# Performance work log

Measured on AMD Instinct MI355X. Metric: run time of the kernel, lower is better.

## Reference

```python
import jax, jax.numpy as jnp
import numpy as np


def _pairwise_sqdist(a, b):
    # a: [B,N,3], b: [B,M,3] -> [B,N,M] squared L2 distances
    a2 = jnp.sum(a * a, axis=-1)            # [B,N]
    b2 = jnp.sum(b * b, axis=-1)            # [B,M]
    ab = jnp.einsum('bnd,bmd->bnm', a, b)   # [B,N,M]
    d = a2[:, :, None] + b2[:, None, :] - 2.0 * ab
    return jnp.maximum(d, 0.0)


def setup_inputs() -> dict:
    key = jax.random.key(0)
    k1, k2 = jax.random.split(key)
    B, N, M = 4, 8192, 8192
    p1 = jax.random.normal(k1, (B, N, 3), dtype=jnp.float32)
    p2 = jax.random.normal(k2, (B, M, 3), dtype=jnp.float32)
    return {"p1": p1, "p2": p2}


def reference(p1, p2):
    # chamfer_3DDist: squared L2 NN distances both directions, then mean of each
    d = _pairwise_sqdist(p1, p2)   # [B,N,M]
    d1 = jnp.min(d, axis=2)        # [B,N] nearest p2 for each p1 point
    d2 = jnp.min(d, axis=1)        # [B,M] nearest p1 for each p2 point
    return jnp.mean(d1) + jnp.mean(d2)
```

## Files before the change

kernel.cpp:

```cpp
#include <hip/hip_runtime.h>
#include <float.h>


typedef float v2f __attribute__((ext_vector_type(2)));
typedef float v4f __attribute__((ext_vector_type(4)));

#define BLK   256
#define QPT   8
#define QPB   (BLK * QPT)
#define BATCH 4
#define NPTS  8192
#define NCH   32
#define CHUNK (NPTS / NCH)
#define QTILES (NPTS / QPB)
#define GRID  (2 * BATCH * QTILES * NCH)
#define TOTQ  (2 * BATCH * NPTS)
#define WS_NEED ((size_t)NCH * TOTQ * sizeof(float))

__global__ void zero_out_kernel(float* out) { out[0] = 0.f; }

__global__ __launch_bounds__(BLK) void cd_chunk_kernel(
    const float* __restrict__ p1, const float* __restrict__ p2,
    float* __restrict__ part)
{
    __shared__ v4f pts[CHUNK];
    int bid    = blockIdx.x;
    int mchunk = bid & (NCH - 1);
    int qt     = (bid >> 5) & (QTILES - 1);
    int batch  = (bid >> 7) & (BATCH - 1);
    int dir    = bid >> 9;

    const float* qbase = (dir == 0 ? p1 : p2) + (size_t)batch * NPTS * 3;
    const float* dbase = (dir == 0 ? p2 : p1) + (size_t)batch * NPTS * 3;

    int tid = threadIdx.x;

    if (tid < CHUNK / 4) {
        int t4 = tid * 4;
        const float* s = dbase + (size_t)(mchunk * CHUNK + t4) * 3;
        float4 f0 = *(const float4*)(s);
        float4 f1 = *(const float4*)(s + 4);
        float4 f2 = *(const float4*)(s + 8);
        float x0 = f0.x, y0 = f0.y, z0 = f0.z;
        float x1 = f0.w, y1 = f1.x, z1 = f1.y;
        float x2 = f1.z, y2 = f1.w, z2 = f2.x;
        float x3 = f2.y, y3 = f2.z, z3 = f2.w;
        float w0 = -0.5f * (x0*x0 + y0*y0 + z0*z0);
        float w1 = -0.5f * (x1*x1 + y1*y1 + z1*z1);
        float w2 = -0.5f * (x2*x2 + y2*y2 + z2*z2);
        float w3 = -0.5f * (x3*x3 + y3*y3 + z3*z3);
        pts[4*tid + 0] = (v4f){x0, x1, y0, y1};
        pts[4*tid + 1] = (v4f){z0, z1, w0, w1};
        pts[4*tid + 2] = (v4f){x2, x3, y2, y3};
        pts[4*tid + 3] = (v4f){z2, z3, w2, w3};
    }

    v2f qx2[QPT], qy2[QPT], qz2[QPT];
    float qn[QPT];
    #pragma unroll
    for (int k = 0; k < QPT; ++k) {
        int q = qt * QPB + k * BLK + tid;
        const float* s = qbase + (size_t)q * 3;
        float qx = s[0], qy = s[1], qz = s[2];
        qx2[k] = (v2f){qx, qx};
        qy2[k] = (v2f){qy, qy};
        qz2[k] = (v2f){qz, qz};
        qn[k] = qx * qx + qy * qy + qz * qz;
    }
    __syncthreads();

    v2f acc0[QPT], acc1[QPT];
    #pragma unroll
    for (int k = 0; k < QPT; ++k) {
        acc0[k] = (v2f){-FLT_MAX, -FLT_MAX};
        acc1[k] = (v2f){-FLT_MAX, -FLT_MAX};
    }

    #pragma unroll 2
    for (int m = 0; m < CHUNK / 2; m += 2) {
        v4f u0 = pts[2*m + 0];
        v4f v0 = pts[2*m + 1];
        v4f u1 = pts[2*m + 2];
        v4f v1 = pts[2*m + 3];
        v2f X0 = __builtin_shufflevector(u0, u0, 0, 1);
        v2f Y0 = __builtin_shufflevector(u0, u0, 2, 3);
        v2f Z0 = __builtin_shufflevector(v0, v0, 0, 1);
        v2f W0 = __builtin_shufflevector(v0, v0, 2, 3);
        v2f X1 = __builtin_shufflevector(u1, u1, 0, 1);
        v2f Y1 = __builtin_shufflevector(u1, u1, 2, 3);
        v2f Z1 = __builtin_shufflevector(v1, v1, 0, 1);
        v2f W1 = __builtin_shufflevector(v1, v1, 2, 3);
        #pragma unroll
        for (int k = 0; k < QPT; ++k) {
            v2f s0 = __builtin_elementwise_fma(qz2[k], Z0,
                      __builtin_elementwise_fma(qy2[k], Y0,
                       __builtin_elementwise_fma(qx2[k], X0, W0)));
            acc0[k] = __builtin_elementwise_max(acc0[k], s0);
            v2f s1 = __builtin_elementwise_fma(qz2[k], Z1,
                      __builtin_elementwise_fma(qy2[k], Y1,
                       __builtin_elementwise_fma(qx2[k], X1, W1)));
            acc1[k] = __builtin_elementwise_max(acc1[k], s1);
        }
    }

    unsigned qid = (unsigned)(dir * (BATCH * NPTS) + batch * NPTS + qt * QPB + tid);
    float* prow = part + (size_t)mchunk * TOTQ;
    #pragma unroll
    for (int k = 0; k < QPT; ++k) {
        float mx = fmaxf(fmaxf(acc0[k].x, acc0[k].y), fmaxf(acc1[k].x, acc1[k].y));
        float d = fmaxf(qn[k] - 2.f * mx, 0.f);
        prow[qid + k * BLK] = d;
    }
}

__global__ __launch_bounds__(BLK) void min_sum_kernel(
    const float* __restrict__ part, float* __restrict__ out, float scale)
{
    int qid = blockIdx.x * BLK + threadIdx.x;
    float v = FLT_MAX;
    #pragma unroll 8
    for (int m = 0; m < NCH; ++m)
        v = fminf(v, part[(size_t)m * TOTQ + qid]);
    for (int off = 32; off > 0; off >>= 1) v += __shfl_down(v, off, 64);
    __shared__ float wsum[BLK / 64];
    int lane = threadIdx.x & 63, wid = threadIdx.x >> 6;
    if (lane == 0) wsum[wid] = v;
    __syncthreads();
    if (threadIdx.x == 0) {
        float t = 0.f;
        for (int w = 0; w < BLK / 64; ++w) t += wsum[w];
        atomicAdd(out, t * scale);
    }
}

__global__ __launch_bounds__(BLK) void init_kernel(unsigned* mins, float* out, int n) {
    int i = blockIdx.x * BLK + threadIdx.x;
    if (i < n) mins[i] = 0x7F7FFFFFu;
    if (i == 0) out[0] = 0.f;
}

__global__ __launch_bounds__(BLK) void cd_chunk_atomic_kernel(
    const float* __restrict__ p1, const float* __restrict__ p2,
    unsigned* __restrict__ mins)
{
    __shared__ v4f pts[CHUNK];
    int bid    = blockIdx.x;
    int mchunk = bid & (NCH - 1);
    int qt     = (bid >> 5) & (QTILES - 1);
    int batch  = (bid >> 7) & (BATCH - 1);
    int dir    = bid >> 9;

    const float* qbase = (dir == 0 ? p1 : p2) + (size_t)batch * NPTS * 3;
    const float* dbase = (dir == 0 ? p2 : p1) + (size_t)batch * NPTS * 3;
    int tid = threadIdx.x;

    if (tid < CHUNK / 4) {
        int t4 = tid * 4;
        const float* s = dbase + (size_t)(mchunk * CHUNK + t4) * 3;
        float4 f0 = *(const float4*)(s);
        float4 f1 = *(const float4*)(s + 4);
        float4 f2 = *(const float4*)(s + 8);
        float x0 = f0.x, y0 = f0.y, z0 = f0.z;
        float x1 = f0.w, y1 = f1.x, z1 = f1.y;
        float x2 = f1.z, y2 = f1.w, z2 = f2.x;
        float x3 = f2.y, y3 = f2.z, z3 = f2.w;
        float w0 = -0.5f * (x0*x0 + y0*y0 + z0*z0);
        float w1 = -0.5f * (x1*x1 + y1*y1 + z1*z1);
        float w2 = -0.5f * (x2*x2 + y2*y2 + z2*z2);
        float w3 = -0.5f * (x3*x3 + y3*y3 + z3*z3);
        pts[4*tid + 0] = (v4f){x0, x1, y0, y1};
        pts[4*tid + 1] = (v4f){z0, z1, w0, w1};
        pts[4*tid + 2] = (v4f){x2, x3, y2, y3};
        pts[4*tid + 3] = (v4f){z2, z3, w2, w3};
    }

    v2f qx2[QPT], qy2[QPT], qz2[QPT];
    float qn[QPT];
    #pragma unroll
    for (int k = 0; k < QPT; ++k) {
        int q = qt * QPB + k * BLK + tid;
        const float* s = qbase + (size_t)q * 3;
        float qx = s[0], qy = s[1], qz = s[2];
        qx2[k] = (v2f){qx, qx}; qy2[k] = (v2f){qy, qy}; qz2[k] = (v2f){qz, qz};
        qn[k] = qx * qx + qy * qy + qz * qz;
    }
    __syncthreads();

    v2f acc0[QPT], acc1[QPT];
    #pragma unroll
    for (int k = 0; k < QPT; ++k) {
        acc0[k] = (v2f){-FLT_MAX, -FLT_MAX};
        acc1[k] = (v2f){-FLT_MAX, -FLT_MAX};
    }
    #pragma unroll 2
    for (int m = 0; m < CHUNK / 2; m += 2) {
        v4f u0 = pts[2*m + 0], v0 = pts[2*m + 1];
        v4f u1 = pts[2*m + 2], v1 = pts[2*m + 3];
        v2f X0 = __builtin_shufflevector(u0, u0, 0, 1);
        v2f Y0 = __builtin_shufflevector(u0, u0, 2, 3);
        v2f Z0 = __builtin_shufflevector(v0, v0, 0, 1);
        v2f W0 = __builtin_shufflevector(v0, v0, 2, 3);
        v2f X1 = __builtin_shufflevector(u1, u1, 0, 1);
        v2f Y1 = __builtin_shufflevector(u1, u1, 2, 3);
        v2f Z1 = __builtin_shufflevector(v1, v1, 0, 1);
        v2f W1 = __builtin_shufflevector(v1, v1, 2, 3);
        #pragma unroll
        for (int k = 0; k < QPT; ++k) {
            v2f s0 = __builtin_elementwise_fma(qz2[k], Z0,
                      __builtin_elementwise_fma(qy2[k], Y0,
                       __builtin_elementwise_fma(qx2[k], X0, W0)));
            acc0[k] = __builtin_elementwise_max(acc0[k], s0);
            v2f s1 = __builtin_elementwise_fma(qz2[k], Z1,
                      __builtin_elementwise_fma(qy2[k], Y1,
                       __builtin_elementwise_fma(qx2[k], X1, W1)));
            acc1[k] = __builtin_elementwise_max(acc1[k], s1);
        }
    }
    unsigned qid = (unsigned)(dir * (BATCH * NPTS) + batch * NPTS + qt * QPB + tid);
    #pragma unroll
    for (int k = 0; k < QPT; ++k) {
        float mx = fmaxf(fmaxf(acc0[k].x, acc0[k].y), fmaxf(acc1[k].x, acc1[k].y));
        float d = fmaxf(qn[k] - 2.f * mx, 0.f);
        atomicMin(&mins[qid + k * BLK], __float_as_uint(d));
    }
}

__global__ __launch_bounds__(BLK) void sum_kernel(
    const unsigned* __restrict__ mins, float* __restrict__ out, int n, float scale)
{
    int i = blockIdx.x * BLK + threadIdx.x;
    int stride = gridDim.x * BLK;
    float v = 0.f;
    for (int idx = i; idx < n; idx += stride) v += __uint_as_float(mins[idx]);
    for (int off = 32; off > 0; off >>= 1) v += __shfl_down(v, off, 64);
    __shared__ float wsum[BLK / 64];
    int lane = threadIdx.x & 63, wid = threadIdx.x >> 6;
    if (lane == 0) wsum[wid] = v;
    __syncthreads();
    if (threadIdx.x == 0) {
        float t = 0.f;
        for (int w = 0; w < BLK / 64; ++w) t += wsum[w];
        atomicAdd(out, t * scale);
    }
}

extern "C" void kernel_launch(void* const* d_in, const int* in_sizes, int n_in,
                              void* d_out, int out_size, void* d_ws, size_t ws_size,
                              hipStream_t stream) {
    const float* p1 = (const float*)d_in[0];
    const float* p2 = (const float*)d_in[1];
    float* out = (float*)d_out;

    if (ws_size >= WS_NEED) {
        float* part = (float*)d_ws;
        zero_out_kernel<<<1, 1, 0, stream>>>(out);
        cd_chunk_kernel<<<GRID, BLK, 0, stream>>>(p1, p2, part);
        min_sum_kernel<<<TOTQ / BLK, BLK, 0, stream>>>(part, out,
                                                       1.f / (float)(BATCH * NPTS));
    } else {
        unsigned* mins = (unsigned*)d_ws;
        init_kernel<<<TOTQ / BLK, BLK, 0, stream>>>(mins, out, TOTQ);
        cd_chunk_atomic_kernel<<<GRID, BLK, 0, stream>>>(p1, p2, mins);
        sum_kernel<<<64, BLK, 0, stream>>>(mins, out, TOTQ, 1.f / (float)(BATCH * NPTS));
    }
}
```

Before: 107.2 us.

## Compute pairwise distance scores with bf16 split-precision MFMA instead of packed FMA

Replaces the packed-FP32 FMA distance loop with a 32x32x16 bf16 MFMA. Each coordinate and the norm term are split into high and low bf16 parts, so one K=16 matrix product approximates the dot product plus the norm offset with near-fp32 accuracy. Query tiles shrink to 128 per block and the database is split into 8 chunks, which also cuts the partial-min workspace and the reduction reads. The cost is bf16 rounding error in the scores, per-tile cross-lane shuffles to reduce the MFMA output, and 16 separate MFMA-max steps per tile.

```diff
diff --git a/kernel.cpp b/kernel.cpp
--- a/kernel.cpp
+++ b/kernel.cpp
@@ -2,42 +2,190 @@
 #include <float.h>
 
 
+typedef short sh8   __attribute__((ext_vector_type(8)));
+typedef float f32x16 __attribute__((ext_vector_type(16)));
+
+#define BLK   256
+#define BATCH 4
+#define NPTS  8192
+#define PCH   8
+#define PCHUNK (NPTS / PCH)
+#define QPB   128
+#define QTILES (NPTS / QPB)
+#define GRID  (2 * BATCH * QTILES * PCH)
+#define TOTQ  (2 * BATCH * NPTS)
+#define WS_NEED ((size_t)PCH * TOTQ * sizeof(float))
+#define ONEBF 0x3F80
+
+__device__ __forceinline__ short f2bf(float f) {
+    unsigned u = __float_as_uint(f);
+    unsigned r = (u + 0x7FFFu + ((u >> 16) & 1u)) >> 16;
+    return (short)r;
+}
+__device__ __forceinline__ float bf2f(short h) {
+    return __uint_as_float(((unsigned)(unsigned short)h) << 16);
+}
+
+__global__ void zero_out_kernel(float* out) { out[0] = 0.f; }
+
+__global__ __launch_bounds__(BLK) void cd_mfma_kernel(
+    const float* __restrict__ p1, const float* __restrict__ p2,
+    float* __restrict__ part)
+{
+    __shared__ uint4 ptsB[PCHUNK * 2];
+
+    int bid    = blockIdx.x;
+    int pchunk = bid & (PCH - 1);
+    int qt     = (bid >> 3) & (QTILES - 1);
+    int batch  = (bid >> 9) & (BATCH - 1);
+    int dir    = bid >> 11;
+
+    const float* qbase = (dir == 0 ? p1 : p2) + (size_t)batch * NPTS * 3;
+    const float* dbase = (dir == 0 ? p2 : p1) + (size_t)batch * NPTS * 3;
+
+    int tid  = threadIdx.x;
+    int wave = tid >> 6;
+    int lane = tid & 63;
+
+    {
+        int t4 = tid * 4;
+        const float* s = dbase + (size_t)(pchunk * PCHUNK + t4) * 3;
+        float4 f0 = *(const float4*)(s);
+        float4 f1 = *(const float4*)(s + 4);
+        float4 f2 = *(const float4*)(s + 8);
+        float px[4] = {f0.x, f0.w, f1.z, f2.y};
+        float py[4] = {f0.y, f1.x, f1.w, f2.z};
+        float pz[4] = {f0.z, f1.y, f2.x, f2.w};
+        #pragma unroll
+        for (int i = 0; i < 4; ++i) {
+            float x = px[i], y = py[i], z = pz[i];
+            short hx = f2bf(x), hy = f2bf(y), hz = f2bf(z);
+            short lx = f2bf(x - bf2f(hx));
+            short ly = f2bf(y - bf2f(hy));
+            short lz = f2bf(z - bf2f(hz));
+            float w = -0.5f * (x * x + y * y + z * z);
+            short wh = f2bf(w);
+            short wl = f2bf(w - bf2f(wh));
+            unsigned uhx = (unsigned short)hx, uhy = (unsigned short)hy, uhz = (unsigned short)hz;
+            unsigned ulx = (unsigned short)lx, uly = (unsigned short)ly, ulz = (unsigned short)lz;
+            ptsB[(t4 + i) * 2 + 0] = make_uint4(
+                uhx | (uhy << 16), uhz | (uhx << 16),
+                uhy | (uhz << 16), ulx | (uly << 16));
+            ptsB[(t4 + i) * 2 + 1] = make_uint4(
+                ulz | (ulx << 16), uly | (ulz << 16),
+                (unsigned)(unsigned short)wh | ((unsigned)(unsigned short)wl << 16),
+                ((unsigned)ONEBF) | (((unsigned)ONEBF) << 16));
+        }
+    }
+
+    sh8 afrag;
+    {
+        int q = qt * QPB + wave * 32 + (lane & 31);
+        const float* s = qbase + (size_t)q * 3;
+        float x = s[0], y = s[1], z = s[2];
+        short hx = f2bf(x), hy = f2bf(y), hz = f2bf(z);
+        short lx = f2bf(x - bf2f(hx));
+        short ly = f2bf(y - bf2f(hy));
+        short lz = f2bf(z - bf2f(hz));
+        float w = -0.5f * (x * x + y * y + z * z);
+        short nh = f2bf(w);
+        short nl = f2bf(w - bf2f(nh));
+        int h = lane >> 5;
+        afrag[0] = h ? hz : hx;
+        afrag[1] = h ? lx : hy;
+        afrag[2] = h ? ly : hz;
+        afrag[3] = h ? lz : lx;
+        afrag[4] = h ? (short)ONEBF : ly;
+        afrag[5] = h ? (short)ONEBF : lz;
+        afrag[6] = h ? nh : hx;
+        afrag[7] = h ? nl : hy;
+    }
+    __syncthreads();
+
+    f32x16 zc;
+    f32x16 runmax;
+    #pragma unroll
+    for (int i = 0; i < 16; ++i) { zc[i] = 0.f; runmax[i] = -FLT_MAX; }
+
+    const sh8* bptr = (const sh8*)ptsB;
+    int boff = (lane & 31) * 2 + (lane >> 5);
+
+    #pragma unroll 4
+    for (int t = 0; t < PCHUNK / 32; ++t) {
+        sh8 bfrag = bptr[t * 64 + boff];
+        f32x16 acc = __builtin_amdgcn_mfma_f32_32x32x16_bf16(afrag, bfrag, zc, 0, 0, 0);
+        runmax = __builtin_elementwise_max(runmax, acc);
+    }
+
+    #pragma unroll
+    for (int step = 1; step <= 16; step <<= 1) {
+        f32x16 o;
+        #pragma unroll
+        for (int i = 0; i < 16; ++i) o[i] = __shfl_xor(runmax[i], step, 64);
+        runmax = __builtin_elementwise_max(runmax, o);
+    }
+
+    if ((lane & 31) == 0) {
+        int half = lane >> 5;
+        int qglob = dir * (BATCH * NPTS) + batch * NPTS + qt * QPB + wave * 32;
+        float* prow = part + (size_t)pchunk * TOTQ + qglob;
+        #pragma unroll
+        for (int reg = 0; reg < 16; ++reg) {
+            int r = (reg & 3) + 8 * (reg >> 2) + 4 * half;
+            float d = fmaxf(-2.f * runmax[reg], 0.f);
+            prow[r] = d;
+        }
+    }
+}
+
+__global__ __launch_bounds__(BLK) void min_sum_kernel(
+    const float* __restrict__ part, float* __restrict__ out, float scale)
+{
+    int qid = blockIdx.x * BLK + threadIdx.x;
+    float v = FLT_MAX;
+    #pragma unroll
+    for (int m = 0; m < PCH; ++m)
+        v = fminf(v, part[(size_t)m * TOTQ + qid]);
+    for (int off = 32; off > 0; off >>= 1) v += __shfl_down(v, off, 64);
+    __shared__ float wsum[BLK / 64];
+    int lane = threadIdx.x & 63, wid = threadIdx.x >> 6;
+    if (lane == 0) wsum[wid] = v;
+    __syncthreads();
+    if (threadIdx.x == 0) {
+        float t = 0.f;
+        for (int w = 0; w < BLK / 64; ++w) t += wsum[w];
+        atomicAdd(out, t * scale);
+    }
+}
+
 typedef float v2f __attribute__((ext_vector_type(2)));
 typedef float v4f __attribute__((ext_vector_type(4)));
-
-#define BLK   256
-#define QPT   8
-#define QPB   (BLK * QPT)
-#define BATCH 4
-#define NPTS  8192
-#define NCH   32
-#define CHUNK (NPTS / NCH)
-#define QTILES (NPTS / QPB)
-#define GRID  (2 * BATCH * QTILES * NCH)
-#define TOTQ  (2 * BATCH * NPTS)
-#define WS_NEED ((size_t)NCH * TOTQ * sizeof(float))
-
-__global__ void zero_out_kernel(float* out) { out[0] = 0.f; }
-
-__global__ __launch_bounds__(BLK) void cd_chunk_kernel(
+#define FQPT   8
+#define FNCH   32
+#define FCHUNK (NPTS / FNCH)
+
+__global__ __launch_bounds__(BLK) void init_kernel(unsigned* mins, float* out, int n) {
+    int i = blockIdx.x * BLK + threadIdx.x;
+    if (i < n) mins[i] = 0x7F7FFFFFu;
+    if (i == 0) out[0] = 0.f;
+}
+
+__global__ __launch_bounds__(BLK) void cd_chunk_atomic_kernel(
     const float* __restrict__ p1, const float* __restrict__ p2,
-    float* __restrict__ part)
-{
-    __shared__ v4f pts[CHUNK];
+    unsigned* __restrict__ mins)
+{
+    __shared__ v4f pts[FCHUNK];
     int bid    = blockIdx.x;
-    int mchunk = bid & (NCH - 1);
-    int qt     = (bid >> 5) & (QTILES - 1);
+    int mchunk = bid & (FNCH - 1);
+    int qt     = (bid >> 5) & 3;
     int batch  = (bid >> 7) & (BATCH - 1);
     int dir    = bid >> 9;
-
     const float* qbase = (dir == 0 ? p1 : p2) + (size_t)batch * NPTS * 3;
     const float* dbase = (dir == 0 ? p2 : p1) + (size_t)batch * NPTS * 3;
-
     int tid = threadIdx.x;
-
-    if (tid < CHUNK / 4) {
+    if (tid < FCHUNK / 4) {
         int t4 = tid * 4;
-        const float* s = dbase + (size_t)(mchunk * CHUNK + t4) * 3;
+        const float* s = dbase + (size_t)(mchunk * FCHUNK + t4) * 3;
         float4 f0 = *(const float4*)(s);
         float4 f1 = *(const float4*)(s + 4);
         float4 f2 = *(const float4*)(s + 8);
@@ -54,146 +202,25 @@
         pts[4*tid + 2] = (v4f){x2, x3, y2, y3};
         pts[4*tid + 3] = (v4f){z2, z3, w2, w3};
     }
-
-    v2f qx2[QPT], qy2[QPT], qz2[QPT];
-    float qn[QPT];
-    #pragma unroll
-    for (int k = 0; k < QPT; ++k) {
-        int q = qt * QPB + k * BLK + tid;
-        const float* s = qbase + (size_t)q * 3;
-        float qx = s[0], qy = s[1], qz = s[2];
-        qx2[k] = (v2f){qx, qx};
-        qy2[k] = (v2f){qy, qy};
-        qz2[k] = (v2f){qz, qz};
-        qn[k] = qx * qx + qy * qy + qz * qz;
-    }
-    __syncthreads();
-
-    v2f acc0[QPT], acc1[QPT];
-    #pragma unroll
-    for (int k = 0; k < QPT; ++k) {
-        acc0[k] = (v2f){-FLT_MAX, -FLT_MAX};
-        acc1[k] = (v2f){-FLT_MAX, -FLT_MAX};
-    }
-
-    #pragma unroll 2
-    for (int m = 0; m < CHUNK / 2; m += 2) {
-        v4f u0 = pts[2*m + 0];
-        v4f v0 = pts[2*m + 1];
-        v4f u1 = pts[2*m + 2];
-        v4f v1 = pts[2*m + 3];
-        v2f X0 = __builtin_shufflevector(u0, u0, 0, 1);
-        v2f Y0 = __builtin_shufflevector(u0, u0, 2, 3);
-        v2f Z0 = __builtin_shufflevector(v0, v0, 0, 1);
-        v2f W0 = __builtin_shufflevector(v0, v0, 2, 3);
-        v2f X1 = __builtin_shufflevector(u1, u1, 0, 1);
-        v2f Y1 = __builtin_shufflevector(u1, u1, 2, 3);
-        v2f Z1 = __builtin_shufflevector(v1, v1, 0, 1);
-        v2f W1 = __builtin_shufflevector(v1, v1, 2, 3);
-        #pragma unroll
-        for (int k = 0; k < QPT; ++k) {
-            v2f s0 = __builtin_elementwise_fma(qz2[k], Z0,
-                      __builtin_elementwise_fma(qy2[k], Y0,
-                       __builtin_elementwise_fma(qx2[k], X0, W0)));
-            acc0[k] = __builtin_elementwise_max(acc0[k], s0);
-            v2f s1 = __builtin_elementwise_fma(qz2[k], Z1,
-                      __builtin_elementwise_fma(qy2[k], Y1,
-                       __builtin_elementwise_fma(qx2[k], X1, W1)));
-            acc1[k] = __builtin_elementwise_max(acc1[k], s1);
-        }
-    }
-
-    unsigned qid = (unsigned)(dir * (BATCH * NPTS) + batch * NPTS + qt * QPB + tid);
-    float* prow = part + (size_t)mchunk * TOTQ;
-    #pragma unroll
-    for (int k = 0; k < QPT; ++k) {
-        float mx = fmaxf(fmaxf(acc0[k].x, acc0[k].y), fmaxf(acc1[k].x, acc1[k].y));
-        float d = fmaxf(qn[k] - 2.f * mx, 0.f);
-        prow[qid + k * BLK] = d;
-    }
-}
-
-__global__ __launch_bounds__(BLK) void min_sum_kernel(
-    const float* __restrict__ part, float* __restrict__ out, float scale)
-{
-    int qid = blockIdx.x * BLK + threadIdx.x;
-    float v = FLT_MAX;
-    #pragma unroll 8
-    for (int m = 0; m < NCH; ++m)
-        v = fminf(v, part[(size_t)m * TOTQ + qid]);
-    for (int off = 32; off > 0; off >>= 1) v += __shfl_down(v, off, 64);
-    __shared__ float wsum[BLK / 64];
-    int lane = threadIdx.x & 63, wid = threadIdx.x >> 6;
-    if (lane == 0) wsum[wid] = v;
-    __syncthreads();
-    if (threadIdx.x == 0) {
-        float t = 0.f;
-        for (int w = 0; w < BLK / 64; ++w) t += wsum[w];
-        atomicAdd(out, t * scale);
-    }
-}
-
-__global__ __launch_bounds__(BLK) void init_kernel(unsigned* mins, float* out, int n) {
-    int i = blockIdx.x * BLK + threadIdx.x;
-    if (i < n) mins[i] = 0x7F7FFFFFu;
-    if (i == 0) out[0] = 0.f;
-}
-
-__global__ __launch_bounds__(BLK) void cd_chunk_atomic_kernel(
-    const float* __restrict__ p1, const float* __restrict__ p2,
-    unsigned* __restrict__ mins)
-{
-    __shared__ v4f pts[CHUNK];
-    int bid    = blockIdx.x;
-    int mchunk = bid & (NCH - 1);
-    int qt     = (bid >> 5) & (QTILES - 1);
-    int batch  = (bid >> 7) & (BATCH - 1);
-    int dir    = bid >> 9;
-
-    const float* qbase = (dir == 0 ? p1 : p2) + (size_t)batch * NPTS * 3;
-    const float* dbase = (dir == 0 ? p2 : p1) + (size_t)batch * NPTS * 3;
-    int tid = threadIdx.x;
-
-    if (tid < CHUNK / 4) {
-        int t4 = tid * 4;
-        const float* s = dbase + (size_t)(mchunk * CHUNK + t4) * 3;
-        float4 f0 = *(const float4*)(s);
-        float4 f1 = *(const float4*)(s + 4);
-        float4 f2 = *(const float4*)(s + 8);
-        float x0 = f0.x, y0 = f0.y, z0 = f0.z;
-        float x1 = f0.w, y1 = f1.x, z1 = f1.y;
-        float x2 = f1.z, y2 = f1.w, z2 = f2.x;
-        float x3 = f2.y, y3 = f2.z, z3 = f2.w;
-        float w0 = -0.5f * (x0*x0 + y0*y0 + z0*z0);
-        float w1 = -0.5f * (x1*x1 + y1*y1 + z1*z1);
-        float w2 = -0.5f * (x2*x2 + y2*y2 + z2*z2);
-        float w3 = -0.5f * (x3*x3 + y3*y3 + z3*z3);
-        pts[4*tid + 0] = (v4f){x0, x1, y0, y1};
-        pts[4*tid + 1] = (v4f){z0, z1, w0, w1};
-        pts[4*tid + 2] = (v4f){x2, x3, y2, y3};
-        pts[4*tid + 3] = (v4f){z2, z3, w2, w3};
-    }
-
-    v2f qx2[QPT], qy2[QPT], qz2[QPT];
-    float qn[QPT];
-    #pragma unroll
-    for (int k = 0; k < QPT; ++k) {
-        int q = qt * QPB + k * BLK + tid;
+    v2f qx2[FQPT], qy2[FQPT], qz2[FQPT];
+    float qn[FQPT];
+    #pragma unroll
+    for (int k = 0; k < FQPT; ++k) {
+        int q = qt * (BLK * FQPT) + k * BLK + tid;
         const float* s = qbase + (size_t)q * 3;
         float qx = s[0], qy = s[1], qz = s[2];
         qx2[k] = (v2f){qx, qx}; qy2[k] = (v2f){qy, qy}; qz2[k] = (v2f){qz, qz};
         qn[k] = qx * qx + qy * qy + qz * qz;
     }
     __syncthreads();
-
-    v2f acc0[QPT], acc1[QPT];
-    #pragma unroll
-    for (int k = 0; k < QPT; ++k) {
+    v2f acc0[FQPT], acc1[FQPT];
+    #pragma unroll
+    for (int k = 0; k < FQPT; ++k) {
         acc0[k] = (v2f){-FLT_MAX, -FLT_MAX};
         acc1[k] = (v2f){-FLT_MAX, -FLT_MAX};
     }
     #pragma unroll 2
-    for (int m = 0; m < CHUNK / 2; m += 2) {
+    for (int m = 0; m < FCHUNK / 2; m += 2) {
         v4f u0 = pts[2*m + 0], v0 = pts[2*m + 1];
         v4f u1 = pts[2*m + 2], v1 = pts[2*m + 3];
         v2f X0 = __builtin_shufflevector(u0, u0, 0, 1);
@@ -205,7 +232,7 @@
         v2f Z1 = __builtin_shufflevector(v1, v1, 0, 1);
         v2f W1 = __builtin_shufflevector(v1, v1, 2, 3);
         #pragma unroll
-        for (int k = 0; k < QPT; ++k) {
+        for (int k = 0; k < FQPT; ++k) {
             v2f s0 = __builtin_elementwise_fma(qz2[k], Z0,
                       __builtin_elementwise_fma(qy2[k], Y0,
                        __builtin_elementwise_fma(qx2[k], X0, W0)));
@@ -216,9 +243,9 @@
             acc1[k] = __builtin_elementwise_max(acc1[k], s1);
         }
     }
-    unsigned qid = (unsigned)(dir * (BATCH * NPTS) + batch * NPTS + qt * QPB + tid);
-    #pragma unroll
-    for (int k = 0; k < QPT; ++k) {
+    unsigned qid = (unsigned)(dir * (BATCH * NPTS) + batch * NPTS + qt * (BLK * FQPT) + tid);
+    #pragma unroll
+    for (int k = 0; k < FQPT; ++k) {
         float mx = fmaxf(fmaxf(acc0[k].x, acc0[k].y), fmaxf(acc1[k].x, acc1[k].y));
         float d = fmaxf(qn[k] - 2.f * mx, 0.f);
         atomicMin(&mins[qid + k * BLK], __float_as_uint(d));
@@ -254,13 +281,13 @@
     if (ws_size >= WS_NEED) {
         float* part = (float*)d_ws;
         zero_out_kernel<<<1, 1, 0, stream>>>(out);
-        cd_chunk_kernel<<<GRID, BLK, 0, stream>>>(p1, p2, part);
+        cd_mfma_kernel<<<GRID, BLK, 0, stream>>>(p1, p2, part);
         min_sum_kernel<<<TOTQ / BLK, BLK, 0, stream>>>(part, out,
                                                        1.f / (float)(BATCH * NPTS));
     } else {
         unsigned* mins = (unsigned*)d_ws;
         init_kernel<<<TOTQ / BLK, BLK, 0, stream>>>(mins, out, TOTQ);
-        cd_chunk_atomic_kernel<<<GRID, BLK, 0, stream>>>(p1, p2, mins);
+        cd_chunk_atomic_kernel<<<1024, BLK, 0, stream>>>(p1, p2, mins);
         sum_kernel<<<64, BLK, 0, stream>>>(mins, out, TOTQ, 1.f / (float)(BATCH * NPTS));
     }
 }
```

Result: slower. 126.6 us (+18.1%).
